# Optimization experiments

Hardware: AMD Instinct MI355X
Metric: run time of the kernel (lower is better)

The kernel has to match this reference:

```python
import jax, jax.numpy as jnp
import numpy as np

GAMMA = 0.1
BATCH, NUM_SV, DIM = 8192, 8192, 256


def setup_inputs() -> dict:
    key = jax.random.key(0)
    k1, k2, k3 = jax.random.split(key, 3)
    x = jax.random.normal(k1, (BATCH, DIM), dtype=jnp.float32)
    support_vectors = jax.random.normal(k2, (NUM_SV, DIM), dtype=jnp.float32)
    dual_coefficients = jax.random.normal(k3, (NUM_SV,), dtype=jnp.float32)
    return {"x": x, "support_vectors": support_vectors, "dual_coefficients": dual_coefficients}


def reference(x, support_vectors, dual_coefficients):
    # Squared Euclidean distance via the GEMM expansion (same math as
    # sum((x[:,None,:]-sv[None,:,:])**2, -1) without the (B, S, D) intermediate).
    x_sq = jnp.sum(x * x, axis=-1, keepdims=True)            # (B, 1)
    sv_sq = jnp.sum(support_vectors * support_vectors, -1)   # (S,)
    cross = jnp.einsum('bd,sd->bs', x, support_vectors)      # (B, S)
    sq_dist = jnp.maximum(x_sq + sv_sq[None, :] - 2.0 * cross, 0.0)
    kernel_matrix = jnp.exp(-GAMMA * sq_dist)                # (B, S)
    return jnp.einsum('bs,s->b', kernel_matrix, dual_coefficients)
```

## Files before the change

### kernel.cpp

```cpp
#include <hip/hip_runtime.h>

#define BATCH 8192
#define NUM_SV 8192
#define DIM 256
#define GAMMA 0.1f
#define LOG2E 1.4426950408889634f
#define ALPHA 0.53715827f

#define SCHUNK 8
#define NST 8
#define NKT 4
#define BTILE_F16 8192

typedef _Float16 f16;
typedef __attribute__((ext_vector_type(8))) _Float16 f16x8;
typedef __attribute__((ext_vector_type(16))) float f32x16;

__global__ __launch_bounds__(256)
void svm_prep(const float* __restrict__ x, const float* __restrict__ sv,
              const float* __restrict__ dual,
              f16* __restrict__ x16, f16* __restrict__ sv16,
              float* __restrict__ xg, float* __restrict__ dcp) {
  const int id = blockIdx.x * 256 + threadIdx.x;
  const bool isx = id < (BATCH * DIM / 8);
  const int lid = isx ? id : id - (BATCH * DIM / 8);
  const int row = lid >> 5;
  const int k0  = (lid & 31) << 3;

  const float* src = (isx ? x : sv) + (size_t)row * DIM + k0;
  float4 u = *(const float4*)(src);
  float4 v = *(const float4*)(src + 4);

  float sq = u.x*u.x + u.y*u.y + u.z*u.z + u.w*u.w
           + v.x*v.x + v.y*v.y + v.z*v.z + v.w*v.w;
  #pragma unroll
  for (int m = 1; m <= 16; m <<= 1) sq += __shfl_xor(sq, m, 32);
  if ((lid & 31) == 0) {
    float g = -(GAMMA * LOG2E) * sq;
    if (isx) xg[row] = g;
    else     dcp[row] = dual[row] * __builtin_amdgcn_exp2f(g);
  }

  f16x8 h;
  h[0] = (f16)(ALPHA * u.x); h[1] = (f16)(ALPHA * u.y);
  h[2] = (f16)(ALPHA * u.z); h[3] = (f16)(ALPHA * u.w);
  h[4] = (f16)(ALPHA * v.x); h[5] = (f16)(ALPHA * v.y);
  h[6] = (f16)(ALPHA * v.z); h[7] = (f16)(ALPHA * v.w);

  if (isx) {
    *(f16x8*)&x16[(size_t)row * DIM + k0] = h;
  } else {
    const int tile = row >> 7;
    const int col  = row & 127;
    const int kt   = k0 >> 6;
    const int ks   = (k0 >> 4) & 3;
    const int kch  = (k0 >> 3) & 1;
    f16* dst = sv16 + (size_t)(tile * NKT + kt) * BTILE_F16
             + ((ks * 2 + kch) * 128 + col) * 8;
    *(f16x8*)dst = h;
  }
}

__global__ __launch_bounds__(256, 2)
void svm_main(const f16* __restrict__ x16, const f16* __restrict__ sv16,
              const float* __restrict__ dcp, float* __restrict__ partial) {
  __shared__ float dcpl[NST * 128];
  __shared__ float red[2][128];

  const int tid = threadIdx.x;
  const int w   = tid >> 6;
  const int l   = tid & 63;
  const int lr  = l & 31;
  const int lh  = l >> 5;
  const int wb  = w >> 1;
  const int wn  = w & 1;

  const int bid = blockIdx.x;
  const int q   = bid & 7;
  const int idx = bid >> 3;
  const int bt  = (q & 3) * 16 + (idx & 15);
  const int sch = (q >> 2) * 4 + (idx >> 4);

  *(float4*)&dcpl[tid * 4] = *(const float4*)&dcp[sch * 1024 + tid * 4];

  f16x8 af[2][16];
  {
    const f16* xb = x16 + (size_t)(bt * 128 + wb * 64 + lr) * DIM + lh * 8;
    #pragma unroll
    for (int m = 0; m < 2; ++m)
      #pragma unroll
      for (int kk = 0; kk < 16; ++kk)
        af[m][kk] = *(const f16x8*)&xb[m * 32 * DIM + kk * 16];
  }
  __syncthreads();

  float ctr[2][16];
  #pragma unroll
  for (int m = 0; m < 2; ++m)
    #pragma unroll
    for (int r = 0; r < 16; ++r) ctr[m][r] = 0.f;

  const int boff = (lh * 128 + wn * 64 + lr) * 8;

  #pragma unroll 1
  for (int st = 0; st < NST; ++st) {
    const f16* bbase = sv16 + (size_t)((sch * NST + st) * NKT) * BTILE_F16 + boff;

    f32x16 acc[2][2];
    #pragma unroll
    for (int m = 0; m < 2; ++m)
      #pragma unroll
      for (int n = 0; n < 2; ++n)
        #pragma unroll
        for (int r = 0; r < 16; ++r) acc[m][n][r] = 0.f;

    #pragma unroll
    for (int kt = 0; kt < NKT; ++kt) {
      const f16* bb = bbase + kt * BTILE_F16;
      #pragma unroll
      for (int ks = 0; ks < 4; ++ks) {
        f16x8 b0 = *(const f16x8*)&bb[ks * 2048];
        f16x8 b1 = *(const f16x8*)&bb[ks * 2048 + 32 * 8];
        acc[0][0] = __builtin_amdgcn_mfma_f32_32x32x16_f16(af[0][kt * 4 + ks], b0, acc[0][0], 0, 0, 0);
        acc[0][1] = __builtin_amdgcn_mfma_f32_32x32x16_f16(af[0][kt * 4 + ks], b1, acc[0][1], 0, 0, 0);
        acc[1][0] = __builtin_amdgcn_mfma_f32_32x32x16_f16(af[1][kt * 4 + ks], b0, acc[1][0], 0, 0, 0);
        acc[1][1] = __builtin_amdgcn_mfma_f32_32x32x16_f16(af[1][kt * 4 + ks], b1, acc[1][1], 0, 0, 0);
      }
    }

    #pragma unroll
    for (int n = 0; n < 2; ++n) {
      const float dv = dcpl[st * 128 + wn * 64 + n * 32 + lr];
      #pragma unroll
      for (int m = 0; m < 2; ++m)
        #pragma unroll
        for (int r = 0; r < 16; ++r)
          ctr[m][r] = fmaf(__builtin_amdgcn_exp2f(acc[m][n][r]), dv, ctr[m][r]);
    }
  }

  #pragma unroll
  for (int m = 0; m < 2; ++m)
    #pragma unroll
    for (int r = 0; r < 16; ++r) {
      float v = ctr[m][r];
      v += __shfl_xor(v, 1, 64);
      v += __shfl_xor(v, 2, 64);
      v += __shfl_xor(v, 4, 64);
      v += __shfl_xor(v, 8, 64);
      v += __shfl_xor(v, 16, 64);
      ctr[m][r] = v;
    }

  __syncthreads();
  if (lr == 0) {
    #pragma unroll
    for (int m = 0; m < 2; ++m)
      #pragma unroll
      for (int r = 0; r < 16; ++r) {
        const int rl = wb * 64 + m * 32 + (r & 3) + 8 * (r >> 2) + 4 * lh;
        red[wn][rl] = ctr[m][r];
      }
  }
  __syncthreads();
  if (tid < 128)
    partial[(size_t)sch * BATCH + bt * 128 + tid] = red[0][tid] + red[1][tid];
}

__global__ __launch_bounds__(256)
void svm_reduce(const float* __restrict__ partial, const float* __restrict__ xg,
                float* __restrict__ out) {
  const int b = blockIdx.x * 256 + threadIdx.x;
  float s = 0.f;
  #pragma unroll
  for (int c = 0; c < SCHUNK; ++c) s += partial[(size_t)c * BATCH + b];
  out[b] = __builtin_amdgcn_exp2f(xg[b]) * s;
}

extern "C" void kernel_launch(void* const* d_in, const int* in_sizes, int n_in,
                              void* d_out, int out_size, void* d_ws, size_t ws_size,
                              hipStream_t stream) {
  const float* x    = (const float*)d_in[0];
  const float* sv   = (const float*)d_in[1];
  const float* dual = (const float*)d_in[2];
  float* out = (float*)d_out;

  f16*   x16     = (f16*)d_ws;
  f16*   sv16    = x16 + (size_t)BATCH * DIM;
  float* xg      = (float*)(sv16 + (size_t)NUM_SV * DIM);
  float* dcp     = xg + BATCH;
  float* partial = dcp + NUM_SV;

  svm_prep<<<(BATCH + NUM_SV) * DIM / 8 / 256, 256, 0, stream>>>(x, sv, dual, x16, sv16, xg, dcp);
  svm_main<<<(BATCH / 128) * SCHUNK, 256, 0, stream>>>(x16, sv16, dcp, partial);
  svm_reduce<<<BATCH / 256, 256, 0, stream>>>(partial, xg, out);
}
```

Measured before the change: 65.64 us.

## Stage support-vector tiles into LDS with async double-buffered global_load_lds

The support-vector fp16 layout is re-tiled into 64-column blocks so each wave can copy its own B tile straight from global memory into a per-wave, double-buffered LDS region with global_load_lds. Loads for step t+2 are issued after the MFMAs of step t, with explicit vmcnt/lgkmcnt waits, so global latency overlaps compute instead of being paid on direct register loads. This adds 64KB of LDS per block, which may limit occupancy at two blocks per CU, and relies on hand-set waitcnt values matching the number of outstanding loads.

```diff
diff --git a/kernel.cpp b/kernel.cpp
--- a/kernel.cpp
+++ b/kernel.cpp
@@ -10,11 +10,16 @@
 #define SCHUNK 8
 #define NST 8
 #define NKT 4
-#define BTILE_F16 8192
+#define NITER (NST * NKT)
 
 typedef _Float16 f16;
 typedef __attribute__((ext_vector_type(8))) _Float16 f16x8;
 typedef __attribute__((ext_vector_type(16))) float f32x16;
+
+__device__ __forceinline__ void gload_lds16(const f16* g, f16* l) {
+  __builtin_amdgcn_global_load_lds((const __attribute__((address_space(1))) void*)g,
+                                   (__attribute__((address_space(3))) void*)l, 16, 0, 0);
+}
 
 __global__ __launch_bounds__(256)
 void svm_prep(const float* __restrict__ x, const float* __restrict__ sv,
@@ -50,13 +55,13 @@
   if (isx) {
     *(f16x8*)&x16[(size_t)row * DIM + k0] = h;
   } else {
-    const int tile = row >> 7;
-    const int col  = row & 127;
-    const int kt   = k0 >> 6;
-    const int ks   = (k0 >> 4) & 3;
-    const int kch  = (k0 >> 3) & 1;
-    f16* dst = sv16 + (size_t)(tile * NKT + kt) * BTILE_F16
-             + ((ks * 2 + kch) * 128 + col) * 8;
+    const int tile64 = row >> 6;
+    const int col    = row & 63;
+    const int kt     = k0 >> 6;
+    const int ks     = (k0 >> 4) & 3;
+    const int kch    = (k0 >> 3) & 1;
+    f16* dst = sv16 + (size_t)((tile64 * NKT + kt) * 8 + ks * 2 + kch) * 512
+             + col * 8;
     *(f16x8*)dst = h;
   }
 }
@@ -64,7 +69,8 @@
 __global__ __launch_bounds__(256, 2)
 void svm_main(const f16* __restrict__ x16, const f16* __restrict__ sv16,
               const float* __restrict__ dcp, float* __restrict__ partial) {
-  __shared__ float dcpl[NST * 128];
+  __shared__ f16 bstage[4][2][4096];
+  __shared__ float dcpl[1024];
   __shared__ float red[2][128];
 
   const int tid = threadIdx.x;
@@ -94,18 +100,27 @@
   }
   __syncthreads();
 
+  auto stage = [&](int t, int par) {
+    const int st = t >> 2, kt = t & 3;
+    const int tile64 = (sch * NST + st) * 2 + wn;
+    const f16* src = sv16 + (size_t)((tile64 * NKT + kt) * 8) * 512 + l * 8;
+    f16* dst = &bstage[w][par][0];
+    #pragma unroll
+    for (int i = 0; i < 8; ++i)
+      gload_lds16(src + i * 512, dst + i * 512);
+  };
+
   float ctr[2][16];
   #pragma unroll
   for (int m = 0; m < 2; ++m)
     #pragma unroll
     for (int r = 0; r < 16; ++r) ctr[m][r] = 0.f;
 
-  const int boff = (lh * 128 + wn * 64 + lr) * 8;
+  stage(0, 0);
+  stage(1, 1);
 
   #pragma unroll 1
   for (int st = 0; st < NST; ++st) {
-    const f16* bbase = sv16 + (size_t)((sch * NST + st) * NKT) * BTILE_F16 + boff;
-
     f32x16 acc[2][2];
     #pragma unroll
     for (int m = 0; m < 2; ++m)
@@ -116,16 +131,26 @@
 
     #pragma unroll
     for (int kt = 0; kt < NKT; ++kt) {
-      const f16* bb = bbase + kt * BTILE_F16;
+      const int t = st * NKT + kt;
+      if (t < NITER - 1)
+        asm volatile("s_waitcnt vmcnt(8)" ::: "memory");
+      else
+        asm volatile("s_waitcnt vmcnt(0)" ::: "memory");
+
+      const f16* buf = &bstage[w][kt & 1][0];
       #pragma unroll
       for (int ks = 0; ks < 4; ++ks) {
-        f16x8 b0 = *(const f16x8*)&bb[ks * 2048];
-        f16x8 b1 = *(const f16x8*)&bb[ks * 2048 + 32 * 8];
+        f16x8 b0 = *(const f16x8*)&buf[(ks * 2 + lh) * 512 + lr * 8];
+        f16x8 b1 = *(const f16x8*)&buf[(ks * 2 + lh) * 512 + (32 + lr) * 8];
         acc[0][0] = __builtin_amdgcn_mfma_f32_32x32x16_f16(af[0][kt * 4 + ks], b0, acc[0][0], 0, 0, 0);
         acc[0][1] = __builtin_amdgcn_mfma_f32_32x32x16_f16(af[0][kt * 4 + ks], b1, acc[0][1], 0, 0, 0);
         acc[1][0] = __builtin_amdgcn_mfma_f32_32x32x16_f16(af[1][kt * 4 + ks], b0, acc[1][0], 0, 0, 0);
         acc[1][1] = __builtin_amdgcn_mfma_f32_32x32x16_f16(af[1][kt * 4 + ks], b1, acc[1][1], 0, 0, 0);
       }
+
+      asm volatile("s_waitcnt lgkmcnt(0)" ::: "memory");
+      __builtin_amdgcn_sched_barrier(0);
+      if (t + 2 < NITER) stage(t + 2, kt & 1);
     }
 
     #pragma unroll
```

After: 60.62 us. -7.6%, faster.
